# Performance work log

Measured on AMD Instinct MI355X. Metric: run time of the kernel, lower is better.

The kernel has to match this reference:

```python
import jax, jax.numpy as jnp
import numpy as np

N = 100000
E = 3200000
NEG_SLOPE = 0.2  # PyG GATConv default


def gat_layer(x, src, dst, W, a_src, a_dst, b, heads, out_ch, concat):
    # per-node linear transform, split into heads: [N, H, C]
    h = (x @ W).reshape(N, heads, out_ch)
    # per-node attention logits: [N, H]
    al_src = jnp.sum(h * a_src, axis=-1)
    al_dst = jnp.sum(h * a_dst, axis=-1)
    # per-edge attention coefficient (x_j = source, x_i = target): [E, H]
    e = jax.nn.leaky_relu(al_src[src] + al_dst[dst], NEG_SLOPE)
    # segment softmax over incoming edges of each destination node
    m = jax.ops.segment_max(e, dst, num_segments=N)
    e = jnp.exp(e - m[dst])
    denom = jax.ops.segment_sum(e, dst, num_segments=N)
    alpha = e / (denom[dst] + 1e-16)
    # weighted message aggregation: scatter-add over dst
    msg = h[src] * alpha[..., None]  # [E, H, C]
    out = jax.ops.segment_sum(msg, dst, num_segments=N)  # [N, H, C]
    out = out.reshape(N, heads * out_ch) if concat else out.mean(axis=1)
    return out + b


def setup_inputs() -> dict:
    key = jax.random.key(0)
    ks = jax.random.split(key, 11)
    return {
        "x": jax.random.normal(ks[0], (N, 2), dtype=jnp.float32),
        "edge_index": jax.random.randint(ks[1], (2, E), 0, N, dtype=jnp.int64),
        "edge_attr": jax.random.normal(ks[2], (E, 1), dtype=jnp.float32),
        "W1": jax.random.normal(ks[3], (2, 32), dtype=jnp.float32) * 0.5,
        "att_src1": jax.random.normal(ks[4], (4, 8), dtype=jnp.float32) * 0.3,
        "att_dst1": jax.random.normal(ks[5], (4, 8), dtype=jnp.float32) * 0.3,
        "b1": jnp.zeros((32,), dtype=jnp.float32),
        "W2": jax.random.normal(ks[6], (32, 2), dtype=jnp.float32) * 0.2,
        "att_src2": jax.random.normal(ks[7], (1, 2), dtype=jnp.float32) * 0.3,
        "att_dst2": jax.random.normal(ks[8], (1, 2), dtype=jnp.float32) * 0.3,
        "b2": jnp.zeros((2,), dtype=jnp.float32),
    }


def reference(x, edge_index, edge_attr, W1, att_src1, att_dst1, b1, W2, att_src2, att_dst2, b2):
    # add self-loops (PyG GATConv default add_self_loops=True)
    loops = jnp.arange(N, dtype=edge_index.dtype)
    src = jnp.concatenate([edge_index[0], loops])
    dst = jnp.concatenate([edge_index[1], loops])
    h = gat_layer(x, src, dst, W1, att_src1, att_dst1, b1, heads=4, out_ch=8, concat=True)
    h = jax.nn.elu(h)
    out = gat_layer(h, src, dst, W2, att_src2, att_dst2, b2, heads=1, out_ch=2, concat=False)
    return out
```

## Files before the change

### kernel.cpp

```cpp
#include <hip/hip_runtime.h>
#include <math.h>

#define NEG_SLOPE 0.2f
#define BK_BITS 8
#define BK (1 << BK_BITS)
#define SBITS 17
#define SMASK ((1 << SBITS) - 1)
#define CAP 9216
#define PPT1 9
#define SW(p) ((p) ^ (((p) >> 5) & 31))

__device__ __forceinline__ float lrelu(float x) { return x > 0.f ? x : NEG_SLOPE * x; }

__global__ void init_bcur(int* __restrict__ bcur, int NB) {
    int i = threadIdx.x;
    if (i < NB) bcur[i] = i * CAP;
}

__global__ __launch_bounds__(512) void bucket_scatter(const int* __restrict__ src,
                                                      const int* __restrict__ dst,
                                                      int* __restrict__ bcur,
                                                      int* __restrict__ pairs, int E) {
    __shared__ int cnt[512], off[512], cur[512], gbase[512];
    __shared__ int lpair[8196];
    __shared__ unsigned short lbkt[8196];
    __shared__ int sTot;
    int t = threadIdx.x;
    cnt[t] = 0;
    __syncthreads();

    int E4 = E >> 2;
    const int4* src4 = (const int4*)src;
    const int4* dst4 = (const int4*)dst;
    int base4 = blockIdx.x * 2048;
    int4 d4[4], s4[4];
    bool val[4];
#pragma unroll
    for (int k = 0; k < 4; k++) {
        int i4 = base4 + k * 512 + t;
        val[k] = (i4 < E4);
        if (val[k]) {
            d4[k] = dst4[i4];
            s4[k] = src4[i4];
            atomicAdd(&cnt[d4[k].x >> BK_BITS], 1);
            atomicAdd(&cnt[d4[k].y >> BK_BITS], 1);
            atomicAdd(&cnt[d4[k].z >> BK_BITS], 1);
            atomicAdd(&cnt[d4[k].w >> BK_BITS], 1);
        }
    }
    int dt = -1, st = 0;
    if (blockIdx.x == gridDim.x - 1) {
        int e = (E4 << 2) + t;
        if (e < E) { dt = dst[e]; st = src[e]; atomicAdd(&cnt[dt >> BK_BITS], 1); }
    }
    __syncthreads();

    if (t < 64) {
        int v[8], mysum = 0;
#pragma unroll
        for (int k = 0; k < 8; k++) { v[k] = cnt[t * 8 + k]; mysum += v[k]; }
        int s = mysum;
#pragma unroll
        for (int o = 1; o < 64; o <<= 1) {
            int u = __shfl_up(s, o);
            if (t >= o) s += u;
        }
        int run = s - mysum;
#pragma unroll
        for (int k = 0; k < 8; k++) {
            int d2 = t * 8 + k;
            off[d2] = run; cur[d2] = run;
            run += v[k];
        }
        if (t == 63) sTot = s;
    }
    __syncthreads();
    if (cnt[t] > 0) gbase[t] = atomicAdd(&bcur[t], cnt[t]);
    __syncthreads();
    int total = sTot;

#pragma unroll
    for (int k = 0; k < 4; k++) {
        if (val[k]) {
            int b, slot;
            b = d4[k].x >> BK_BITS; slot = atomicAdd(&cur[b], 1);
            lpair[slot] = ((d4[k].x & (BK - 1)) << SBITS) | s4[k].x; lbkt[slot] = (unsigned short)b;
            b = d4[k].y >> BK_BITS; slot = atomicAdd(&cur[b], 1);
            lpair[slot] = ((d4[k].y & (BK - 1)) << SBITS) | s4[k].y; lbkt[slot] = (unsigned short)b;
            b = d4[k].z >> BK_BITS; slot = atomicAdd(&cur[b], 1);
            lpair[slot] = ((d4[k].z & (BK - 1)) << SBITS) | s4[k].z; lbkt[slot] = (unsigned short)b;
            b = d4[k].w >> BK_BITS; slot = atomicAdd(&cur[b], 1);
            lpair[slot] = ((d4[k].w & (BK - 1)) << SBITS) | s4[k].w; lbkt[slot] = (unsigned short)b;
        }
    }
    if (dt >= 0) {
        int b = dt >> BK_BITS;
        int slot = atomicAdd(&cur[b], 1);
        lpair[slot] = ((dt & (BK - 1)) << SBITS) | st; lbkt[slot] = (unsigned short)b;
    }
    __syncthreads();

    for (int i = t; i < total; i += 512) {
        int b = lbkt[i];
        pairs[gbase[b] + (i - off[b])] = lpair[i];
    }
}

__global__ __launch_bounds__(1024) void agg1_sortgather(
        const int* __restrict__ pairs, const int* __restrict__ bcur,
        const float2* __restrict__ x2,
        const float* __restrict__ W1, const float* __restrict__ asrc,
        const float* __restrict__ adst, const float* __restrict__ b1,
        const float* __restrict__ W2, const float* __restrict__ as2,
        const float* __restrict__ ad2,
        float2* __restrict__ h2, float* __restrict__ al2d,
        int* __restrict__ rowdeg, int* __restrict__ pairs_out, int N) {
    __shared__ float sW[64], sB[32], sW2[64], sP[4], sQ[4], sPd[4], sQd[4], sA2[4];
    __shared__ int cnt[BK], off[BK], cur[BK];
    __shared__ int sorted[CAP];
    int t = threadIdx.x;
    int b = blockIdx.x;
    if (t < 64) { sW[t] = W1[t]; sW2[t] = W2[t]; }
    if (t < 32) sB[t] = b1[t];
    if (t < 2) { sA2[t] = as2[t]; sA2[2 + t] = ad2[t]; }
    if (t >= 64 && t < 68) {
        int tt = t - 64;
        float P = 0.f, Q = 0.f, Pd = 0.f, Qd = 0.f;
#pragma unroll
        for (int k = 0; k < 8; k++) {
            int c = tt * 8 + k;
            float a = asrc[c], ad_ = adst[c];
            float w0 = W1[c], w1 = W1[32 + c];
            P += w0 * a; Q += w1 * a;
            Pd += w0 * ad_; Qd += w1 * ad_;
        }
        sP[tt] = P; sQ[tt] = Q; sPd[tt] = Pd; sQd[tt] = Qd;
    }
    if (t < BK) cnt[t] = 0;
    __syncthreads();

    int dbase = b << BK_BITS;
    int ndst = min(BK, N - dbase);
    int lo = b * CAP;
    int hi = min(bcur[b], lo + CAP);

    int myp[PPT1];
#pragma unroll
    for (int k = 0; k < PPT1; k++) {
        int i = lo + t + k * 1024;
        int p = (i < hi) ? pairs[i] : -1;
        myp[k] = p;
        if (p >= 0) atomicAdd(&cnt[p >> SBITS], 1);
    }
    __syncthreads();

    if (t < 64) {
        int v[4], mysum = 0;
#pragma unroll
        for (int k = 0; k < 4; k++) { v[k] = cnt[t * 4 + k]; mysum += v[k]; }
        int s = mysum;
#pragma unroll
        for (int o = 1; o < 64; o <<= 1) {
            int u = __shfl_up(s, o);
            if (t >= o) s += u;
        }
        int run = s - mysum;
#pragma unroll
        for (int k = 0; k < 4; k++) {
            int d2 = t * 4 + k;
            off[d2] = run; cur[d2] = run;
            run += v[k];
        }
    }
    __syncthreads();

#pragma unroll
    for (int k = 0; k < PPT1; k++) {
        int p = myp[k];
        if (p >= 0) {
            int pos = atomicAdd(&cur[p >> SBITS], 1);
            sorted[SW(pos)] = p & SMASK;
        }
    }
    __syncthreads();

    {
        const int4* s4 = (const int4*)sorted;
        int4* p4 = (int4*)(pairs_out + lo);
        for (int i = t; i < CAP / 4; i += 1024) p4[i] = s4[i];
    }
    if (t < ndst) rowdeg[dbase + t] = (off[t] << 8) | min(cnt[t], 255);

    int d = t >> 2, q = t & 3;
    if (d < ndst) {
        int n = dbase + d;
        float rP[4], rQ[4], ald[4];
        float2 xd = x2[n];
#pragma unroll
        for (int h = 0; h < 4; h++) {
            rP[h] = sP[h]; rQ[h] = sQ[h];
            ald[h] = xd.x * sPd[h] + xd.y * sQd[h];
        }
        int deg = cnt[d];
        int start = off[d];
        float Sw[4] = {0.f, 0.f, 0.f, 0.f};
        float S0[4] = {0.f, 0.f, 0.f, 0.f};
        float S1[4] = {0.f, 0.f, 0.f, 0.f};
        for (int j = q; j < deg; j += 8) {
            int s0 = sorted[SW(start + j)];
            int s1 = (j + 4 < deg) ? sorted[SW(start + j + 4)] : -1;
            float2 x0 = x2[s0];
            float2 x1 = (s1 >= 0) ? x2[s1] : make_float2(0.f, 0.f);
#pragma unroll
            for (int h = 0; h < 4; h++) {
                float e = lrelu(fmaf(x0.x, rP[h], fmaf(x0.y, rQ[h], ald[h])));
                float w = __expf(fminf(e, 80.f));
                Sw[h] += w; S0[h] += w * x0.x; S1[h] += w * x0.y;
            }
            if (s1 >= 0) {
#pragma unroll
                for (int h = 0; h < 4; h++) {
                    float e = lrelu(fmaf(x1.x, rP[h], fmaf(x1.y, rQ[h], ald[h])));
                    float w = __expf(fminf(e, 80.f));
                    Sw[h] += w; S0[h] += w * x1.x; S1[h] += w * x1.y;
                }
            }
        }
#pragma unroll
        for (int o = 1; o <= 2; o <<= 1) {
#pragma unroll
            for (int h = 0; h < 4; h++) {
                Sw[h] += __shfl_xor(Sw[h], o);
                S0[h] += __shfl_xor(S0[h], o);
                S1[h] += __shfl_xor(S1[h], o);
            }
        }
        if (q == 0) {
#pragma unroll
            for (int h = 0; h < 4; h++) {
                float e = lrelu(fmaf(xd.x, rP[h], fmaf(xd.y, rQ[h], ald[h])));
                float w = __expf(fminf(e, 80.f));
                Sw[h] += w; S0[h] += w * xd.x; S1[h] += w * xd.y;
            }
            float r[4];
#pragma unroll
            for (int h = 0; h < 4; h++) r[h] = 1.f / (Sw[h] + 1e-16f);
            float h20 = 0.f, h21 = 0.f;
#pragma unroll
            for (int c = 0; c < 32; c++) {
                int h = c >> 3;
                float outc = (sW[c] * S0[h] + sW[32 + c] * S1[h]) * r[h];
                float v2 = outc + sB[c];
                v2 = v2 > 0.f ? v2 : __expf(v2) - 1.f;
                h20 = fmaf(v2, sW2[2 * c], h20);
                h21 = fmaf(v2, sW2[2 * c + 1], h21);
            }
            h2[n] = make_float2(h20, h21);
            al2d[n] = h20 * sA2[2] + h21 * sA2[3];
        }
    }
}

__global__ __launch_bounds__(1024) void agg2_gather(
        const int* __restrict__ pairs, const int* __restrict__ rowdeg,
        const float2* __restrict__ h2, const float* __restrict__ al2d,
        const float* __restrict__ as2, const float* __restrict__ b2,
        float2* __restrict__ out, int N) {
    __shared__ int sorted[CAP];
    int t = threadIdx.x;
    int b = blockIdx.x;
    int dbase = b << BK_BITS;
    int ndst = min(BK, N - dbase);
    int lo = b * CAP;
    float a0 = as2[0], a1 = as2[1];

    {
        const int4* p4 = (const int4*)(pairs + lo);
        int4* s4 = (int4*)sorted;
        for (int i = t; i < CAP / 4; i += 1024) s4[i] = p4[i];
    }
    __syncthreads();

    int d = t >> 2, q = t & 3;
    if (d < ndst) {
        int n = dbase + d;
        int rd = rowdeg[n];
        int start = rd >> 8;
        int deg = rd & 255;
        float ald = al2d[n];
        float2 hd = h2[n];
        float wsum = 0.f, ax = 0.f, ay = 0.f;
        for (int j = q; j < deg; j += 8) {
            int s0 = sorted[SW(start + j)];
            int s1 = (j + 4 < deg) ? sorted[SW(start + j + 4)] : -1;
            float2 v0 = h2[s0];
            float2 v1 = (s1 >= 0) ? h2[s1] : make_float2(0.f, 0.f);
            float e0 = lrelu(fmaf(v0.x, a0, fmaf(v0.y, a1, ald)));
            float w0 = __expf(fminf(e0, 80.f));
            wsum += w0; ax = fmaf(w0, v0.x, ax); ay = fmaf(w0, v0.y, ay);
            if (s1 >= 0) {
                float e1 = lrelu(fmaf(v1.x, a0, fmaf(v1.y, a1, ald)));
                float w1 = __expf(fminf(e1, 80.f));
                wsum += w1; ax = fmaf(w1, v1.x, ax); ay = fmaf(w1, v1.y, ay);
            }
        }
#pragma unroll
        for (int o = 1; o <= 2; o <<= 1) {
            wsum += __shfl_xor(wsum, o);
            ax += __shfl_xor(ax, o);
            ay += __shfl_xor(ay, o);
        }
        if (q == 0) {
            float e = lrelu(fmaf(hd.x, a0, fmaf(hd.y, a1, ald)));
            float w = __expf(fminf(e, 80.f));
            wsum += w; ax = fmaf(w, hd.x, ax); ay = fmaf(w, hd.y, ay);
            float inv = 1.f / (wsum + 1e-16f);
            out[n] = make_float2(ax * inv + b2[0], ay * inv + b2[1]);
        }
    }
}

extern "C" void kernel_launch(void* const* d_in, const int* in_sizes, int n_in,
                              void* d_out, int out_size, void* d_ws, size_t ws_size,
                              hipStream_t stream) {
    const float* x     = (const float*)d_in[0];
    const int*   eidx  = (const int*)d_in[1];
    const float* W1    = (const float*)d_in[3];
    const float* asrc1 = (const float*)d_in[4];
    const float* adst1 = (const float*)d_in[5];
    const float* b1    = (const float*)d_in[6];
    const float* W2    = (const float*)d_in[7];
    const float* asrc2 = (const float*)d_in[8];
    const float* adst2 = (const float*)d_in[9];
    const float* b2    = (const float*)d_in[10];

    const int N = in_sizes[0] / 2;
    const int E = in_sizes[1] / 2;
    const int* src = eidx;
    const int* dst = eidx + E;
    const int NB = (N + BK - 1) >> BK_BITS;

    float* w = (float*)d_ws;
    float2* h2    = (float2*)w;
    float*  al2d  = w + 2 * (size_t)N;
    int* ip       = (int*)(w + 3 * (size_t)N);
    int* rowdeg   = ip;
    int* bcur     = ip + (size_t)N;
    int* pairs    = ip + (size_t)N + 512;

    int E4 = E >> 2;
    int gS = (E4 + 2047) / 2048;

    init_bcur<<<1, 512, 0, stream>>>(bcur, NB);
    bucket_scatter<<<gS, 512, 0, stream>>>(src, dst, bcur, pairs, E);
    agg1_sortgather<<<NB, 1024, 0, stream>>>(pairs, bcur, (const float2*)x,
                                             W1, asrc1, adst1, b1, W2, asrc2, adst2,
                                             h2, al2d, rowdeg, pairs, N);
    agg2_gather<<<NB, 1024, 0, stream>>>(pairs, rowdeg, (const float2*)h2, al2d,
                                         asrc2, b2, (float2*)d_out, N);
}
```

Measured before the change: 159.9 us.

## Batch neighbor gathers for memory-level parallelism and simplify bucket scatter staging

The aggregation kernels now preload up to 16 neighbor ids per thread and issue 8 independent x2/h2 gathers at a time before computing, replacing the old 2-at-a-time loop. A scalar tail loop handles degrees above 64. The intent is to hide global gather latency through more loads in flight. Bucket scatter issues all global loads before the shared atomics, keeps raw (dst,src) int2 pairs in LDS, and folds the global base into one adjusted offset. This removes the separate bucket-id array and a subtraction, at the cost of more registers and LDS.

```diff
diff --git a/kernel.cpp b/kernel.cpp
--- a/kernel.cpp
+++ b/kernel.cpp
@@ -21,9 +21,8 @@
                                                       const int* __restrict__ dst,
                                                       int* __restrict__ bcur,
                                                       int* __restrict__ pairs, int E) {
-    __shared__ int cnt[512], off[512], cur[512], gbase[512];
-    __shared__ int lpair[8196];
-    __shared__ unsigned short lbkt[8196];
+    __shared__ int cnt[512], off[512], cur[512], adj[512];
+    __shared__ int2 lpair[8196];
     __shared__ int sTot;
     int t = threadIdx.x;
     cnt[t] = 0;
@@ -39,20 +38,23 @@
     for (int k = 0; k < 4; k++) {
         int i4 = base4 + k * 512 + t;
         val[k] = (i4 < E4);
+        if (val[k]) { d4[k] = dst4[i4]; s4[k] = src4[i4]; }
+    }
+    int dt = -1, st = 0;
+    if (blockIdx.x == gridDim.x - 1) {
+        int e = (E4 << 2) + t;
+        if (e < E) { dt = dst[e]; st = src[e]; }
+    }
+#pragma unroll
+    for (int k = 0; k < 4; k++) {
         if (val[k]) {
-            d4[k] = dst4[i4];
-            s4[k] = src4[i4];
             atomicAdd(&cnt[d4[k].x >> BK_BITS], 1);
             atomicAdd(&cnt[d4[k].y >> BK_BITS], 1);
             atomicAdd(&cnt[d4[k].z >> BK_BITS], 1);
             atomicAdd(&cnt[d4[k].w >> BK_BITS], 1);
         }
     }
-    int dt = -1, st = 0;
-    if (blockIdx.x == gridDim.x - 1) {
-        int e = (E4 << 2) + t;
-        if (e < E) { dt = dst[e]; st = src[e]; atomicAdd(&cnt[dt >> BK_BITS], 1); }
-    }
+    if (dt >= 0) atomicAdd(&cnt[dt >> BK_BITS], 1);
     __syncthreads();
 
     if (t < 64) {
@@ -75,34 +77,33 @@
         if (t == 63) sTot = s;
     }
     __syncthreads();
-    if (cnt[t] > 0) gbase[t] = atomicAdd(&bcur[t], cnt[t]);
+    if (cnt[t] > 0) {
+        int g = atomicAdd(&bcur[t], cnt[t]);
+        adj[t] = g - off[t];
+    }
     __syncthreads();
     int total = sTot;
 
 #pragma unroll
     for (int k = 0; k < 4; k++) {
         if (val[k]) {
-            int b, slot;
-            b = d4[k].x >> BK_BITS; slot = atomicAdd(&cur[b], 1);
-            lpair[slot] = ((d4[k].x & (BK - 1)) << SBITS) | s4[k].x; lbkt[slot] = (unsigned short)b;
-            b = d4[k].y >> BK_BITS; slot = atomicAdd(&cur[b], 1);
-            lpair[slot] = ((d4[k].y & (BK - 1)) << SBITS) | s4[k].y; lbkt[slot] = (unsigned short)b;
-            b = d4[k].z >> BK_BITS; slot = atomicAdd(&cur[b], 1);
-            lpair[slot] = ((d4[k].z & (BK - 1)) << SBITS) | s4[k].z; lbkt[slot] = (unsigned short)b;
-            b = d4[k].w >> BK_BITS; slot = atomicAdd(&cur[b], 1);
-            lpair[slot] = ((d4[k].w & (BK - 1)) << SBITS) | s4[k].w; lbkt[slot] = (unsigned short)b;
+            int slot;
+            slot = atomicAdd(&cur[d4[k].x >> BK_BITS], 1); lpair[slot] = make_int2(d4[k].x, s4[k].x);
+            slot = atomicAdd(&cur[d4[k].y >> BK_BITS], 1); lpair[slot] = make_int2(d4[k].y, s4[k].y);
+            slot = atomicAdd(&cur[d4[k].z >> BK_BITS], 1); lpair[slot] = make_int2(d4[k].z, s4[k].z);
+            slot = atomicAdd(&cur[d4[k].w >> BK_BITS], 1); lpair[slot] = make_int2(d4[k].w, s4[k].w);
         }
     }
     if (dt >= 0) {
-        int b = dt >> BK_BITS;
-        int slot = atomicAdd(&cur[b], 1);
-        lpair[slot] = ((dt & (BK - 1)) << SBITS) | st; lbkt[slot] = (unsigned short)b;
+        int slot = atomicAdd(&cur[dt >> BK_BITS], 1);
+        lpair[slot] = make_int2(dt, st);
     }
     __syncthreads();
 
     for (int i = t; i < total; i += 512) {
-        int b = lbkt[i];
-        pairs[gbase[b] + (i - off[b])] = lpair[i];
+        int2 e = lpair[i];
+        int b = e.x >> BK_BITS;
+        pairs[adj[b] + i] = ((e.x & (BK - 1)) << SBITS) | e.y;
     }
 }
 
@@ -148,9 +149,11 @@
 #pragma unroll
     for (int k = 0; k < PPT1; k++) {
         int i = lo + t + k * 1024;
-        int p = (i < hi) ? pairs[i] : -1;
-        myp[k] = p;
-        if (p >= 0) atomicAdd(&cnt[p >> SBITS], 1);
+        myp[k] = (i < hi) ? pairs[i] : -1;
+    }
+#pragma unroll
+    for (int k = 0; k < PPT1; k++) {
+        if (myp[k] >= 0) atomicAdd(&cnt[myp[k] >> SBITS], 1);
     }
     __syncthreads();
 
@@ -203,27 +206,43 @@
         }
         int deg = cnt[d];
         int start = off[d];
+        int ids[16];
+#pragma unroll
+        for (int k = 0; k < 16; k++) {
+            int j = q + 4 * k;
+            ids[k] = (j < deg) ? sorted[SW(start + j)] : -1;
+        }
         float Sw[4] = {0.f, 0.f, 0.f, 0.f};
         float S0[4] = {0.f, 0.f, 0.f, 0.f};
         float S1[4] = {0.f, 0.f, 0.f, 0.f};
-        for (int j = q; j < deg; j += 8) {
-            int s0 = sorted[SW(start + j)];
-            int s1 = (j + 4 < deg) ? sorted[SW(start + j + 4)] : -1;
-            float2 x0 = x2[s0];
-            float2 x1 = (s1 >= 0) ? x2[s1] : make_float2(0.f, 0.f);
+#pragma unroll
+        for (int half = 0; half < 2; half++) {
+            float2 xv[8];
+#pragma unroll
+            for (int k = 0; k < 8; k++) {
+                int id = ids[half * 8 + k];
+                xv[k] = x2[id >= 0 ? id : 0];
+            }
+#pragma unroll
+            for (int k = 0; k < 8; k++) {
+                if (ids[half * 8 + k] >= 0) {
+#pragma unroll
+                    for (int h = 0; h < 4; h++) {
+                        float e = lrelu(fmaf(xv[k].x, rP[h], fmaf(xv[k].y, rQ[h], ald[h])));
+                        float w = __expf(fminf(e, 80.f));
+                        Sw[h] += w; S0[h] += w * xv[k].x; S1[h] += w * xv[k].y;
+                    }
+                }
+            }
+        }
+        for (int j = q + 64; j < deg; j += 4) {
+            int s = sorted[SW(start + j)];
+            float2 xs = x2[s];
 #pragma unroll
             for (int h = 0; h < 4; h++) {
-                float e = lrelu(fmaf(x0.x, rP[h], fmaf(x0.y, rQ[h], ald[h])));
+                float e = lrelu(fmaf(xs.x, rP[h], fmaf(xs.y, rQ[h], ald[h])));
                 float w = __expf(fminf(e, 80.f));
-                Sw[h] += w; S0[h] += w * x0.x; S1[h] += w * x0.y;
-            }
-            if (s1 >= 0) {
-#pragma unroll
-                for (int h = 0; h < 4; h++) {
-                    float e = lrelu(fmaf(x1.x, rP[h], fmaf(x1.y, rQ[h], ald[h])));
-                    float w = __expf(fminf(e, 80.f));
-                    Sw[h] += w; S0[h] += w * x1.x; S1[h] += w * x1.y;
-                }
+                Sw[h] += w; S0[h] += w * xs.x; S1[h] += w * xs.y;
             }
         }
 #pragma unroll
@@ -289,20 +308,36 @@
         int deg = rd & 255;
         float ald = al2d[n];
         float2 hd = h2[n];
+        int ids[16];
+#pragma unroll
+        for (int k = 0; k < 16; k++) {
+            int j = q + 4 * k;
+            ids[k] = (j < deg) ? sorted[SW(start + j)] : -1;
+        }
         float wsum = 0.f, ax = 0.f, ay = 0.f;
-        for (int j = q; j < deg; j += 8) {
-            int s0 = sorted[SW(start + j)];
-            int s1 = (j + 4 < deg) ? sorted[SW(start + j + 4)] : -1;
-            float2 v0 = h2[s0];
-            float2 v1 = (s1 >= 0) ? h2[s1] : make_float2(0.f, 0.f);
-            float e0 = lrelu(fmaf(v0.x, a0, fmaf(v0.y, a1, ald)));
-            float w0 = __expf(fminf(e0, 80.f));
-            wsum += w0; ax = fmaf(w0, v0.x, ax); ay = fmaf(w0, v0.y, ay);
-            if (s1 >= 0) {
-                float e1 = lrelu(fmaf(v1.x, a0, fmaf(v1.y, a1, ald)));
-                float w1 = __expf(fminf(e1, 80.f));
-                wsum += w1; ax = fmaf(w1, v1.x, ax); ay = fmaf(w1, v1.y, ay);
-            }
+#pragma unroll
+        for (int half = 0; half < 2; half++) {
+            float2 hv[8];
+#pragma unroll
+            for (int k = 0; k < 8; k++) {
+                int id = ids[half * 8 + k];
+                hv[k] = h2[id >= 0 ? id : 0];
+            }
+#pragma unroll
+            for (int k = 0; k < 8; k++) {
+                if (ids[half * 8 + k] >= 0) {
+                    float e = lrelu(fmaf(hv[k].x, a0, fmaf(hv[k].y, a1, ald)));
+                    float w = __expf(fminf(e, 80.f));
+                    wsum += w; ax = fmaf(w, hv[k].x, ax); ay = fmaf(w, hv[k].y, ay);
+                }
+            }
+        }
+        for (int j = q + 64; j < deg; j += 4) {
+            int s = sorted[SW(start + j)];
+            float2 hv = h2[s];
+            float e = lrelu(fmaf(hv.x, a0, fmaf(hv.y, a1, ald)));
+            float w = __expf(fminf(e, 80.f));
+            wsum += w; ax = fmaf(w, hv.x, ax); ay = fmaf(w, hv.y, ay);
         }
 #pragma unroll
         for (int o = 1; o <= 2; o <<= 1) {
```

After: 160.1 us. About the same (+0.2%).
